# Kernel tuning notes

Measured on AMD Instinct MI355X. Metric: run time of the kernel, lower is better.

Reference implementation:

```python
import jax, jax.numpy as jnp
import numpy as np

ALPHA = 0.1
MAX_ITER = 35
TOL = 0.01
STEP = ALPHA / 2.0  # step_size = alpha/2 as in TV2DFunction.forward


def _prox_tv1d(step, y):
    """Exact 1D TV prox via taut-string lower/upper hulls (faithful port of _prox_tv1d)."""
    n = y.shape[0]
    width = n + 1
    dt = y.dtype
    cs = jnp.cumsum(y)
    y_low = jnp.concatenate([jnp.zeros(1, dt), cs - step]).at[width - 1].add(step)
    y_up = jnp.concatenate([jnp.zeros(1, dt), cs + step]).at[width - 1].add(-step)

    inf = jnp.asarray(jnp.inf, dt)
    il = jnp.zeros(width, jnp.int32)   # index_low
    iu = jnp.zeros(width, jnp.int32)   # index_up
    idx = jnp.zeros(width, jnp.int32)  # breakpoint indices
    sl = jnp.zeros(width, dt).at[0].set(inf)    # slope_low
    su = jnp.zeros(width, dt).at[0].set(-inf)   # slope_up
    z = jnp.zeros(width, dt)
    zero = jnp.int32(0)

    def fdiv(num, a, b):
        # a > b always holds on the taken branch; maximum() only guards the
        # unselected jnp.where branch against NaN/Inf.
        return num / jnp.maximum(a - b, 1).astype(dt)

    def body(i, st):
        il, sl, iu, su, idx, z, s_l, c_l, s_u, c_u, c = st
        c_l = c_l + 1
        c_u = c_u + 1
        il = il.at[c_l].set(i)
        iu = iu.at[c_u].set(i)
        sl = sl.at[c_l].set(y_low[i] - y_low[i - 1])

        def w1_cond(t):
            il_, sl_, c_l_ = t
            return (c_l_ > s_l + 1) & (sl_[jnp.maximum(s_l, c_l_ - 1)] <= sl_[c_l_])

        def w1_body(t):
            il_, sl_, c_l_ = t
            c_l_ = c_l_ - 1
            il_ = il_.at[c_l_].set(i)
            ns = jnp.where(c_l_ > s_l + 1,
                           fdiv(y_low[i] - y_low[il_[c_l_ - 1]], i, il_[c_l_ - 1]),
                           fdiv(y_low[i] - z[c], i, idx[c]))
            return il_, sl_.at[c_l_].set(ns), c_l_

        il, sl, c_l = jax.lax.while_loop(w1_cond, w1_body, (il, sl, c_l))

        su = su.at[c_u].set(y_up[i] - y_up[i - 1])

        def w2_cond(t):
            iu_, su_, c_u_ = t
            return (c_u_ > s_u + 1) & (su_[jnp.maximum(s_u, c_u_ - 1)] >= su_[c_u_])

        def w2_body(t):
            iu_, su_, c_u_ = t
            c_u_ = c_u_ - 1
            iu_ = iu_.at[c_u_].set(i)
            ns = jnp.where(c_u_ > s_u + 1,
                           fdiv(y_up[i] - y_up[iu_[c_u_ - 1]], i, iu_[c_u_ - 1]),
                           fdiv(y_up[i] - z[c], i, idx[c]))
            return iu_, su_.at[c_u_].set(ns), c_u_

        iu, su, c_u = jax.lax.while_loop(w2_cond, w2_body, (iu, su, c_u))

        def w3_cond(t):
            idx_, z_, sl_, il_, s_u_, c_ = t
            return (c_l == s_l + 1) & (c_u > s_u_ + 1) & (sl_[c_l] >= su[s_u_ + 1])

        def w3_body(t):
            idx_, z_, sl_, il_, s_u_, c_ = t
            c_ = c_ + 1
            s_u_ = s_u_ + 1
            k = iu[s_u_]
            idx_ = idx_.at[c_].set(k)
            z_ = z_.at[c_].set(y_up[k])
            il_ = il_.at[s_l].set(k)
            sl_ = sl_.at[c_l].set(fdiv(y_low[i] - y_up[k], i, k))
            return idx_, z_, sl_, il_, s_u_, c_

        idx, z, sl, il, s_u, c = jax.lax.while_loop(w3_cond, w3_body, (idx, z, sl, il, s_u, c))

        def w4_cond(t):
            idx_, z_, su_, iu_, s_l_, c_ = t
            return (c_u == s_u + 1) & (c_l > s_l_ + 1) & (su_[c_u] <= sl[s_l_ + 1])

        def w4_body(t):
            idx_, z_, su_, iu_, s_l_, c_ = t
            c_ = c_ + 1
            s_l_ = s_l_ + 1
            k = il[s_l_]
            idx_ = idx_.at[c_].set(k)
            z_ = z_.at[c_].set(y_low[k])
            iu_ = iu_.at[s_u].set(k)
            su_ = su_.at[c_u].set(fdiv(y_up[i] - y_low[k], i, k))
            return idx_, z_, su_, iu_, s_l_, c_

        idx, z, su, iu, s_l, c = jax.lax.while_loop(w4_cond, w4_body, (idx, z, su, iu, s_l, c))

        return il, sl, iu, su, idx, z, s_l, c_l, s_u, c_u, c

    st = (il, sl, iu, su, idx, z, zero, zero, zero, zero, zero)
    il, sl, iu, su, idx, z, s_l, c_l, s_u, c_u, c = jax.lax.fori_loop(1, width, body, st)

    # tail: append remaining lower-hull points to the breakpoint list
    m = c_l - s_l
    offs = jnp.arange(width)
    valid = (offs >= 1) & (offs <= m)
    src = il[jnp.clip(s_l + offs, 0, width - 1)]
    tgt = jnp.where(valid, c + offs, width)  # 'width' is out of bounds -> dropped
    idx = idx.at[tgt].set(src, mode='drop')
    z = z.at[tgt].set(y_low[src], mode='drop')
    c = c + m

    # piecewise-constant output: slope of taut string on each segment
    a = (z - jnp.roll(z, 1)) / jnp.maximum(idx - jnp.roll(idx, 1), 1).astype(dt)
    knots = jnp.where(offs <= c, idx, n + 1)  # sorted; idx[c] == n
    seg = jnp.searchsorted(knots, jnp.arange(n), side='right')  # segment id in [1, c]
    return a[seg]


def _prox_cols(step, A):
    return jax.vmap(lambda col: _prox_tv1d(step, col), in_axes=1, out_axes=1)(A)


def _prox_rows(step, A):
    return jax.vmap(lambda row: _prox_tv1d(step, row))(A)


def _prox_tv2d(x, step, max_iter, tol):
    """Douglas-Rachford splitting for 2D TV prox (Barbero & Sra 2014)."""
    def cond(carry):
        it, x_, p, q, acc = carry
        return (it < max_iter) & (acc >= tol)

    def body(carry):
        it, x_, p, q, _ = carry
        y = _prox_cols(step, x_ + p)
        p = p + x_ - y
        x2 = _prox_rows(step, y + q)
        q = q + y - x2
        acc = jnp.max(jnp.abs(y - x2))
        return it + 1, x2, p, q, acc

    z0 = jnp.zeros_like(x)
    init = (jnp.int32(0), x, z0, z0, jnp.asarray(jnp.inf, x.dtype))
    return jax.lax.while_loop(cond, body, init)[1]


def setup_inputs() -> dict:
    key = jax.random.key(0)
    X = jax.random.normal(key, (256, 256), dtype=jnp.float32)
    return {"X": X}


def reference(X):
    return _prox_tv2d(X, STEP, MAX_ITER, TOL)
```

## Files before the change

### kernel.cpp

```cpp
#include <hip/hip_runtime.h>

#define N 256
#define NLINE 4
#define NB (N / NLINE)
#define NT (NLINE * 64)
#define LAM 0.05f
#define TWOLAM (2.0f * LAM)
#define FOURLAM (4.0f * LAM)
#define MAXIT 35
#define TOL 0.01f
#define SLOTSTRIDE 16

__device__ __forceinline__ float rlane(float v, int lane) {
    return __int_as_float(__builtin_amdgcn_readlane(__float_as_int(v), lane));
}

__device__ __forceinline__ void gstore(float* p, float v) {
    __hip_atomic_store(p, v, __ATOMIC_RELAXED, __HIP_MEMORY_SCOPE_AGENT);
}
__device__ __forceinline__ float4 gload4(const float* p) {
    float4 r;
    asm volatile("global_load_dwordx4 %0, %1, off sc0 sc1\n\ts_waitcnt vmcnt(0)"
                 : "=&v"(r) : "v"(p) : "memory");
    return r;
}

struct Dist { float r0, r1, r2, r3; };

__device__ __forceinline__ float dfetch(const Dist& d, int k) {
    const int lane = k & 63;
    const int sel = k >> 6;
    float a = rlane(d.r0, lane);
    float b = rlane(d.r1, lane);
    float c = rlane(d.r2, lane);
    float e = rlane(d.r3, lane);
    float ab = (sel & 1) ? b : a;
    float ce = (sel & 1) ? e : c;
    return (sel & 2) ? ce : ab;
}

__device__ __forceinline__ void flushseg(Dist& o, int lo, int hi, float val, int lane) {
    const unsigned len = (unsigned)(hi - lo);
    const int base = lane - lo;
    o.r0 = ((unsigned)(base      ) <= len) ? val : o.r0;
    o.r1 = ((unsigned)(base + 64 ) <= len) ? val : o.r1;
    o.r2 = ((unsigned)(base + 128) <= len) ? val : o.r2;
    o.r3 = ((unsigned)(base + 192) <= len) ? val : o.r3;
}

__device__ __forceinline__ unsigned long long sel4(unsigned long long a, unsigned long long b,
                                                   unsigned long long c, unsigned long long d, int r) {
    unsigned long long ab = (r & 1) ? b : a;
    unsigned long long cd = (r & 1) ? d : c;
    return (r & 2) ? cd : ab;
}

__device__ void tv1d_scan(const Dist& v, Dist& o, const int lane)
{
    const float lam = LAM, mlam = -LAM, twolam = TWOLAM;

    Dist vnx;
    {
        float a0 = __shfl_down(v.r0, 1), a1 = __shfl_down(v.r1, 1);
        float a2 = __shfl_down(v.r2, 1), a3 = __shfl_down(v.r3, 1);
        const bool hi = (lane == 63);
        vnx.r0 = hi ? rlane(v.r1, 0) : a0;
        vnx.r1 = hi ? rlane(v.r2, 0) : a1;
        vnx.r2 = hi ? rlane(v.r3, 0) : a2;
        vnx.r3 = hi ? v.r3 : a3;
    }
    Dist d;
    d.r0 = vnx.r0 - v.r0;  d.r1 = vnx.r1 - v.r1;
    d.r2 = vnx.r2 - v.r2;  d.r3 = vnx.r3 - v.r3;
    const unsigned lambits = __float_as_uint(lam);
    Dist sl;
    sl.r0 = __uint_as_float((__float_as_uint(d.r0) & 0x80000000u) | lambits);
    sl.r1 = __uint_as_float((__float_as_uint(d.r1) & 0x80000000u) | lambits);
    sl.r2 = __uint_as_float((__float_as_uint(d.r2) & 0x80000000u) | lambits);
    sl.r3 = __uint_as_float((__float_as_uint(d.r3) & 0x80000000u) | lambits);
    Dist slp;
    {
        float b0 = __shfl_up(sl.r0, 1), b1 = __shfl_up(sl.r1, 1);
        float b2 = __shfl_up(sl.r2, 1), b3 = __shfl_up(sl.r3, 1);
        const bool lo = (lane == 0);
        slp.r0 = lo ? 0.0f : b0;
        slp.r1 = lo ? rlane(sl.r0, 63) : b1;
        slp.r2 = lo ? rlane(sl.r1, 63) : b2;
        slp.r3 = lo ? rlane(sl.r2, 63) : b3;
    }
    Dist e, g;
    {
        float t0 = v.r0 - slp.r0, t1 = v.r1 - slp.r1, t2 = v.r2 - slp.r2, t3 = v.r3 - slp.r3;
        e.r0 = t0 + sl.r0;  e.r1 = t1 + sl.r1;  e.r2 = t2 + sl.r2;  e.r3 = t3 + sl.r3;
        g.r0 = t0 - lam;    g.r1 = t1 - lam;    g.r2 = t2 - lam;    g.r3 = t3 - lam;
    }
    const unsigned long long S0 = __ballot(d.r0 < 0.0f);
    const unsigned long long S1 = __ballot(d.r1 < 0.0f);
    const unsigned long long S2 = __ballot(d.r2 < 0.0f);
    const unsigned long long S3 = __ballot(d.r3 < 0.0f);
    const unsigned long long B20 = __ballot(fabsf(d.r0) > TWOLAM);
    const unsigned long long B21 = __ballot(fabsf(d.r1) > TWOLAM);
    const unsigned long long B22 = __ballot(fabsf(d.r2) > TWOLAM);
    const unsigned long long B23 = __ballot(fabsf(d.r3) > TWOLAM);
    const unsigned long long B40 = __ballot(fabsf(d.r0) > FOURLAM);
    const unsigned long long B41 = __ballot(fabsf(d.r1) > FOURLAM);
    const unsigned long long B42 = __ballot(fabsf(d.r2) > FOURLAM);
    const unsigned long long B43 = __ballot(fabsf(d.r3) > FOURLAM);
    const unsigned long long Sp0 = (S0 << 1);
    const unsigned long long Sp1 = (S1 << 1) | (S0 >> 63);
    const unsigned long long Sp2 = (S2 << 1) | (S1 >> 63);
    const unsigned long long Sp3 = (S3 << 1) | (S2 >> 63);
    const unsigned long long NF0 = ~(B40 | (B20 & ~(S0 ^ Sp0)));
    const unsigned long long NF1 = ~(B41 | (B21 & ~(S1 ^ Sp1)));
    const unsigned long long NF2 = ~(B42 | (B22 & ~(S2 ^ Sp2)));
    const unsigned long long NF3 = ~((B43 | (B23 & ~(S3 ^ Sp3))) & 0x7FFFFFFFFFFFFFFFull);
    const unsigned long long FNn0 = (S0 & B20) | (~S0 & B40);
    const unsigned long long FNn1 = (S1 & B21) | (~S1 & B41);
    const unsigned long long FNn2 = (S2 & B22) | (~S2 & B42);
    const unsigned long long FNn3 = (S3 & B23) | (~S3 & B43);
    const unsigned long long FNp0 = (~S0 & B20) | (S0 & B40);
    const unsigned long long FNp1 = (~S1 & B21) | (S1 & B41);
    const unsigned long long FNp2 = (~S2 & B22) | (S2 & B42);
    const unsigned long long FNp3 = (~S3 & B23) | (S3 & B43);
    const int initFF = (int)(B40 & 1ull);

    auto firstnf = [&](int jmin) -> int {
        const int w = jmin >> 6;
        unsigned long long m = sel4(NF0, NF1, NF2, NF3, w) >> (jmin & 63);
        if (m) return jmin + (int)__builtin_ctzll(m);
        unsigned long long m1 = (w < 1) ? NF1 : 0ull;
        unsigned long long m2 = (w < 2) ? NF2 : 0ull;
        if (m1) return 64 + (int)__builtin_ctzll(m1);
        if (m2) return 128 + (int)__builtin_ctzll(m2);
        return 192 + (int)__builtin_ctzll(NF3);
    };

    auto trigbit = [&](int kk, int neg) -> int {
        const int w = kk >> 6;
        const unsigned long long m = neg ? sel4(FNn0, FNn1, FNn2, FNn3, w)
                                         : sel4(FNp0, FNp1, FNp2, FNp3, w);
        return (int)((m >> (kk & 63)) & 1ull);
    };

    int k = 0, k0 = 0, km = 0, kp = 0;
    float umin = lam, umax = mlam;
    const float v0 = rlane(v.r0, 0);
    float vmin = v0 - lam, vmax = v0 + lam;
    float flen = 1.0f;
    float rnext = 0.5f;
    float vn1 = rlane(vnx.r0, 0);

    auto fastfwd = [&]() {
        const int K1 = firstnf(k + 1);
        const int sneg = (int)((sel4(S0, S1, S2, S3, k >> 6) >> (k & 63)) & 1ull);
        flushseg(o, k, k, sneg ? vmin : vmax, lane);
        if (K1 > k + 1) {
            const int lo = k + 1;
            const unsigned len = (unsigned)(K1 - 1 - lo);
            const int base = lane - lo;
            o.r0 = ((unsigned)(base      ) <= len) ? e.r0 : o.r0;
            o.r1 = ((unsigned)(base + 64 ) <= len) ? e.r1 : o.r1;
            o.r2 = ((unsigned)(base + 128) <= len) ? e.r2 : o.r2;
            o.r3 = ((unsigned)(base + 192) <= len) ? e.r3 : o.r3;
        }
        k = K1; k0 = K1; km = K1; kp = K1;
        vmin = dfetch(g, K1);
        vmax = vmin + twolam;
        umin = lam; umax = mlam;
        flen = 1.0f; rnext = 0.5f;
        vn1 = dfetch(vnx, K1);
    };

    auto do_step = [&]() {
        const float un = umin + vn1 - vmin;
        const float ux = umax + vn1 - vmax;
        const bool neg = un < mlam;
        const bool pos = ux > lam;
        const int wn = (k + 1) >> 6, bn = (k + 1) & 63;
        const int tn = (int)((sel4(FNn0, FNn1, FNn2, FNn3, wn) >> bn) & 1ull);
        const int tp = (int)((sel4(FNp0, FNp1, FNp2, FNp3, wn) >> bn) & 1ull);
        if (__builtin_expect((int)(neg | pos), 1)) {
            const float fval = neg ? vmin : vmax;
            const int   fhi  = neg ? km : kp;
            flushseg(o, k0, fhi, fval, lane);
            const int k0n = fhi + 1;
            float vstar;
            int trig;
            if (__builtin_expect((int)(k0n <= k), 0)) {
                vstar = dfetch(v, k0n);
                trig = trigbit(k0n, (int)neg);
            } else {
                vstar = vn1;
                trig = neg ? tn : tp;
            }
            k = k0n; k0 = k0n; km = k0n; kp = k0n;
            vmin = neg ? vstar : vstar - twolam;
            vmax = vmin + twolam;
            umin = lam; umax = mlam;
            flen = 1.0f; rnext = 0.5f;
            if (k < N - 1 && trig) {
                fastfwd();
            } else {
                vn1 = dfetch(vnx, k);
            }
        } else {
            k++;
            const float r = rnext;
            flen += 1.0f;
            const bool cmin = (un >= lam);
            const bool cmax = (ux <= mlam);
            vmin = cmin ? fmaf(un - lam, r, vmin) : vmin;
            km   = cmin ? k : km;
            umin = cmin ? lam : un;
            vmax = cmax ? fmaf(ux + lam, r, vmax) : vmax;
            kp   = cmax ? k : kp;
            umax = cmax ? mlam : ux;
            vn1 = dfetch(vnx, k);
            rnext = __builtin_amdgcn_rcpf(flen + 1.0f);
        }
    };

    if (initFF) fastfwd();

    for (;;) {
        while (k < N - 1) {
            do_step();
            if (k >= N - 1) break;
            do_step();
        }
        for (;;) {
            if (umin < 0.0f) {
                flushseg(o, k0, km, vmin, lane);
                k0 = km + 1;
                if (k0 > N - 1) return;
                km = k = k0;
                vmin = dfetch(v, k0);
                umin = lam;
                umax = vmin + lam - vmax;
                flen = 1.0f;
            } else if (umax > 0.0f) {
                flushseg(o, k0, kp, vmax, lane);
                k0 = kp + 1;
                if (k0 > N - 1) return;
                kp = k = k0;
                vmax = dfetch(v, k0);
                umax = mlam;
                umin = vmax - lam - vmin;
                flen = 1.0f;
            } else {
                vmin += umin / flen;
                flushseg(o, k0, k, vmin, lane);
                return;
            }
            if (k != N - 1) break;
        }
        rnext = 0.5f;
        vn1 = dfetch(vnx, k);
    }
}

__device__ __forceinline__ void gridbar1(unsigned long long* slots, unsigned seq,
                                         unsigned accfill, int t) {
    __syncthreads();
    __builtin_amdgcn_s_waitcnt(0);
    if (t == 0)
        __hip_atomic_store(&slots[blockIdx.x * SLOTSTRIDE],
                           ((unsigned long long)accfill << 32) | (unsigned long long)seq,
                           __ATOMIC_RELAXED, __HIP_MEMORY_SCOPE_AGENT);
    if (t < 64) {
        unsigned long long f = __hip_atomic_load(&slots[t * SLOTSTRIDE],
                                                 __ATOMIC_RELAXED, __HIP_MEMORY_SCOPE_AGENT);
        for (;;) {
            unsigned long long fn = __hip_atomic_load(&slots[t * SLOTSTRIDE],
                                                      __ATOMIC_RELAXED, __HIP_MEMORY_SCOPE_AGENT);
            if (__all((int)((unsigned)f >= seq))) break;
            f = fn;
        }
    }
    __syncthreads();
}

__device__ __forceinline__ void gridbar2(unsigned long long* slots, unsigned seq,
                                         unsigned acc, int t, int* s_dec) {
    __syncthreads();
    __builtin_amdgcn_s_waitcnt(0);
    if (t == 0)
        __hip_atomic_store(&slots[blockIdx.x * SLOTSTRIDE],
                           ((unsigned long long)acc << 32) | (unsigned long long)seq,
                           __ATOMIC_RELAXED, __HIP_MEMORY_SCOPE_AGENT);
    if (t < 64) {
        unsigned long long f = __hip_atomic_load(&slots[t * SLOTSTRIDE],
                                                 __ATOMIC_RELAXED, __HIP_MEMORY_SCOPE_AGENT);
        for (;;) {
            unsigned long long fn = __hip_atomic_load(&slots[t * SLOTSTRIDE],
                                                      __ATOMIC_RELAXED, __HIP_MEMORY_SCOPE_AGENT);
            if (__all((int)((unsigned)f >= seq))) break;
            f = fn;
        }
        unsigned a = (unsigned)(f >> 32);
        #pragma unroll
        for (int off = 32; off > 0; off >>= 1) {
            unsigned aa = __shfl_xor(a, off);
            a = (aa > a) ? aa : a;
        }
        if (t == 0) *s_dec = (__uint_as_float(a) < TOL) ? 1 : 0;
    }
    __syncthreads();
}

__global__ __launch_bounds__(NT) void tv2d_coop(const float* __restrict__ X,
                                                float* __restrict__ xw,
                                                float* __restrict__ y,
                                                unsigned long long* __restrict__ slots)
{
    const int t = threadIdx.x;
    const int lane = t & 63;
    const int wave = t >> 6;
    const int line = blockIdx.x * NLINE + wave;
    const int col4 = 4 * blockIdx.x;
    __shared__ float tile[N * 5];
    __shared__ unsigned s_acc;
    __shared__ int s_dec;
    if (t == 0) s_acc = 0u;

    Dist p = {0.f, 0.f, 0.f, 0.f};
    Dist q = {0.f, 0.f, 0.f, 0.f};
    unsigned accprev = 0u;

    for (int it = 0; it < MAXIT; ++it) {
        const float* xs = (it == 0) ? X : xw;
        const float4 xc = gload4(xs + t * N + col4);
        tile[t * 5 + 0] = xc.x;
        tile[t * 5 + 1] = xc.y;
        tile[t * 5 + 2] = xc.z;
        tile[t * 5 + 3] = xc.w;
        __syncthreads();
        Dist v, o;
        v.r0 = tile[(lane      ) * 5 + wave] + p.r0;
        v.r1 = tile[(lane + 64 ) * 5 + wave] + p.r1;
        v.r2 = tile[(lane + 128) * 5 + wave] + p.r2;
        v.r3 = tile[(lane + 192) * 5 + wave] + p.r3;
        tv1d_scan(v, o, lane);
        p.r0 = v.r0 - o.r0;  p.r1 = v.r1 - o.r1;
        p.r2 = v.r2 - o.r2;  p.r3 = v.r3 - o.r3;
        float* yt = y + line * N;
        gstore(yt + lane,       o.r0);
        gstore(yt + lane + 64,  o.r1);
        gstore(yt + lane + 128, o.r2);
        gstore(yt + lane + 192, o.r3);
        gridbar1(slots, 2u * (unsigned)it + 1u, accprev, t);

        const float4 yc = gload4(y + t * N + col4);
        tile[t * 5 + 0] = yc.x;
        tile[t * 5 + 1] = yc.y;
        tile[t * 5 + 2] = yc.z;
        tile[t * 5 + 3] = yc.w;
        __syncthreads();
        float y0 = tile[(lane      ) * 5 + wave];
        float y1 = tile[(lane + 64 ) * 5 + wave];
        float y2 = tile[(lane + 128) * 5 + wave];
        float y3 = tile[(lane + 192) * 5 + wave];
        Dist w, o2;
        w.r0 = y0 + q.r0;
        w.r1 = y1 + q.r1;
        w.r2 = y2 + q.r2;
        w.r3 = y3 + q.r3;
        tv1d_scan(w, o2, lane);
        float d0 = y0 - o2.r0;
        float d1 = y1 - o2.r1;
        float d2 = y2 - o2.r2;
        float d3 = y3 - o2.r3;
        q.r0 = w.r0 - o2.r0;  q.r1 = w.r1 - o2.r1;
        q.r2 = w.r2 - o2.r2;  q.r3 = w.r3 - o2.r3;
        float* xr = xw + line * N;
        gstore(xr + lane,       o2.r0);
        gstore(xr + lane + 64,  o2.r1);
        gstore(xr + lane + 128, o2.r2);
        gstore(xr + lane + 192, o2.r3);

        float am = fmaxf(fmaxf(fabsf(d0), fabsf(d1)), fmaxf(fabsf(d2), fabsf(d3)));
        #pragma unroll
        for (int off = 32; off > 0; off >>= 1)
            am = fmaxf(am, __shfl_xor(am, off));
        if (lane == 0) atomicMax(&s_acc, __float_as_uint(am));
        __syncthreads();
        const unsigned ba = s_acc;

        if (it == MAXIT - 1) break;

        gridbar2(slots, 2u * (unsigned)it + 2u, ba, t, &s_dec);
        if (t == 0) s_acc = 0u;
        if (s_dec) break;
        accprev = ba;
    }
}

extern "C" void kernel_launch(void* const* d_in, const int* in_sizes, int n_in,
                              void* d_out, int out_size, void* d_ws, size_t ws_size,
                              hipStream_t stream) {
    const float* X = (const float*)d_in[0];
    float* xw = (float*)d_out;
    float* y = (float*)d_ws;
    unsigned long long* slots = (unsigned long long*)((char*)d_ws + (size_t)N * N * sizeof(float));
    (void)hipMemsetAsync((void*)slots, 0, NB * SLOTSTRIDE * sizeof(unsigned long long), stream);
    void* args[] = { (void*)&X, (void*)&xw, (void*)&y, (void*)&slots };
    (void)hipLaunchCooperativeKernel((void*)tv2d_coop, dim3(NB), dim3(NT), args, 0, stream);
}
```

Measured before the change: 285.2 us.

## Replace block-level grid barriers with per-wave slots, DPP reductions, prefetched scan loads

Each wave now publishes its own slot in the grid barrier. Wave 0 polls all 256 slots and releases the other waves of its block through a shared-memory flag, instead of the barrier being wrapped in two __syncthreads. The per-wave max reductions switch from shuffle loops to DPP row operations plus a readlane, which removes the shared atomicMax and a block sync. The scan step also computes the next-element register selects for all three branch targets up front, to shorten the dependency chain after the branch. The cost is more slot polling traffic per wave and extra select work on every scan step.

```diff
diff --git a/kernel.cpp b/kernel.cpp
--- a/kernel.cpp
+++ b/kernel.cpp
@@ -9,7 +9,7 @@
 #define FOURLAM (4.0f * LAM)
 #define MAXIT 35
 #define TOL 0.01f
-#define SLOTSTRIDE 16
+#define SLOTSTRIDE 4
 
 __device__ __forceinline__ float rlane(float v, int lane) {
     return __int_as_float(__builtin_amdgcn_readlane(__float_as_int(v), lane));
@@ -53,6 +53,17 @@
     unsigned long long ab = (r & 1) ? b : a;
     unsigned long long cd = (r & 1) ? d : c;
     return (r & 2) ? cd : ab;
+}
+
+__device__ __forceinline__ unsigned wredmax(unsigned x) {
+    unsigned t;
+    t = (unsigned)__builtin_amdgcn_update_dpp(0, (int)x, 0x111, 0xf, 0xf, true); x = x > t ? x : t;
+    t = (unsigned)__builtin_amdgcn_update_dpp(0, (int)x, 0x112, 0xf, 0xf, true); x = x > t ? x : t;
+    t = (unsigned)__builtin_amdgcn_update_dpp(0, (int)x, 0x114, 0xf, 0xf, true); x = x > t ? x : t;
+    t = (unsigned)__builtin_amdgcn_update_dpp(0, (int)x, 0x118, 0xf, 0xf, true); x = x > t ? x : t;
+    t = (unsigned)__builtin_amdgcn_update_dpp(0, (int)x, 0x142, 0xf, 0xf, true); x = x > t ? x : t;
+    t = (unsigned)__builtin_amdgcn_update_dpp(0, (int)x, 0x143, 0xf, 0xf, true); x = x > t ? x : t;
+    return (unsigned)__builtin_amdgcn_readlane((int)x, 63);
 }
 
 __device__ void tv1d_scan(const Dist& v, Dist& o, const int lane)
@@ -172,6 +183,9 @@
     };
 
     auto do_step = [&]() {
+        const float pf_nj = dfetch(vnx, k + 1);
+        const float pf_n  = dfetch(vnx, km + 1);
+        const float pf_p  = dfetch(vnx, kp + 1);
         const float un = umin + vn1 - vmin;
         const float ux = umax + vn1 - vmax;
         const bool neg = un < mlam;
@@ -201,7 +215,7 @@
             if (k < N - 1 && trig) {
                 fastfwd();
             } else {
-                vn1 = dfetch(vnx, k);
+                vn1 = neg ? pf_n : pf_p;
             }
         } else {
             k++;
@@ -215,7 +229,7 @@
             vmax = cmax ? fmaf(ux + lam, r, vmax) : vmax;
             kp   = cmax ? k : kp;
             umax = cmax ? mlam : ux;
-            vn1 = dfetch(vnx, k);
+            vn1 = pf_nj;
             rnext = __builtin_amdgcn_rcpf(flen + 1.0f);
         }
     };
@@ -259,53 +273,48 @@
     }
 }
 
-__device__ __forceinline__ void gridbar1(unsigned long long* slots, unsigned seq,
-                                         unsigned accfill, int t) {
-    __syncthreads();
+template <bool WANT>
+__device__ __forceinline__ unsigned wavebar(unsigned long long* slots, unsigned seq,
+                                            unsigned payload, int line, int lane, int wave,
+                                            unsigned long long* s_rel)
+{
     __builtin_amdgcn_s_waitcnt(0);
-    if (t == 0)
-        __hip_atomic_store(&slots[blockIdx.x * SLOTSTRIDE],
-                           ((unsigned long long)accfill << 32) | (unsigned long long)seq,
-                           __ATOMIC_RELAXED, __HIP_MEMORY_SCOPE_AGENT);
-    if (t < 64) {
-        unsigned long long f = __hip_atomic_load(&slots[t * SLOTSTRIDE],
-                                                 __ATOMIC_RELAXED, __HIP_MEMORY_SCOPE_AGENT);
+    __hip_atomic_store(&slots[line * SLOTSTRIDE],
+                       ((unsigned long long)payload << 32) | (unsigned long long)seq,
+                       __ATOMIC_RELAXED, __HIP_MEMORY_SCOPE_AGENT);
+    unsigned ga = 0u;
+    if (wave == 0) {
+        auto ld = [&](int i) {
+            return __hip_atomic_load(&slots[i * SLOTSTRIDE],
+                                     __ATOMIC_RELAXED, __HIP_MEMORY_SCOPE_AGENT);
+        };
+        unsigned long long f0 = ld(lane), f1 = ld(lane + 64),
+                           f2 = ld(lane + 128), f3 = ld(lane + 192);
         for (;;) {
-            unsigned long long fn = __hip_atomic_load(&slots[t * SLOTSTRIDE],
-                                                      __ATOMIC_RELAXED, __HIP_MEMORY_SCOPE_AGENT);
-            if (__all((int)((unsigned)f >= seq))) break;
-            f = fn;
-        }
-    }
-    __syncthreads();
-}
-
-__device__ __forceinline__ void gridbar2(unsigned long long* slots, unsigned seq,
-                                         unsigned acc, int t, int* s_dec) {
-    __syncthreads();
-    __builtin_amdgcn_s_waitcnt(0);
-    if (t == 0)
-        __hip_atomic_store(&slots[blockIdx.x * SLOTSTRIDE],
-                           ((unsigned long long)acc << 32) | (unsigned long long)seq,
-                           __ATOMIC_RELAXED, __HIP_MEMORY_SCOPE_AGENT);
-    if (t < 64) {
-        unsigned long long f = __hip_atomic_load(&slots[t * SLOTSTRIDE],
-                                                 __ATOMIC_RELAXED, __HIP_MEMORY_SCOPE_AGENT);
-        for (;;) {
-            unsigned long long fn = __hip_atomic_load(&slots[t * SLOTSTRIDE],
-                                                      __ATOMIC_RELAXED, __HIP_MEMORY_SCOPE_AGENT);
-            if (__all((int)((unsigned)f >= seq))) break;
-            f = fn;
-        }
-        unsigned a = (unsigned)(f >> 32);
-        #pragma unroll
-        for (int off = 32; off > 0; off >>= 1) {
-            unsigned aa = __shfl_xor(a, off);
-            a = (aa > a) ? aa : a;
-        }
-        if (t == 0) *s_dec = (__uint_as_float(a) < TOL) ? 1 : 0;
-    }
-    __syncthreads();
+            unsigned long long g0 = ld(lane), g1 = ld(lane + 64),
+                               g2 = ld(lane + 128), g3 = ld(lane + 192);
+            const bool ok = ((unsigned)f0 >= seq) & ((unsigned)f1 >= seq) &
+                            ((unsigned)f2 >= seq) & ((unsigned)f3 >= seq);
+            if (__all((int)ok)) break;
+            f0 = g0; f1 = g1; f2 = g2; f3 = g3;
+        }
+        if (WANT) {
+            unsigned a = (unsigned)(f0 >> 32), b = (unsigned)(f1 >> 32);
+            unsigned c = (unsigned)(f2 >> 32), d = (unsigned)(f3 >> 32);
+            a = a > b ? a : b;  c = c > d ? c : d;  a = a > c ? a : c;
+            ga = wredmax(a);
+        }
+        if (lane == 0)
+            __hip_atomic_store(s_rel, ((unsigned long long)ga << 32) | (unsigned long long)seq,
+                               __ATOMIC_RELAXED, __HIP_MEMORY_SCOPE_WORKGROUP);
+    } else {
+        unsigned long long r;
+        do {
+            r = __hip_atomic_load(s_rel, __ATOMIC_RELAXED, __HIP_MEMORY_SCOPE_WORKGROUP);
+        } while ((unsigned)r < seq);
+        if (WANT) ga = (unsigned)(r >> 32);
+    }
+    return ga;
 }
 
 __global__ __launch_bounds__(NT) void tv2d_coop(const float* __restrict__ X,
@@ -319,9 +328,8 @@
     const int line = blockIdx.x * NLINE + wave;
     const int col4 = 4 * blockIdx.x;
     __shared__ float tile[N * 5];
-    __shared__ unsigned s_acc;
-    __shared__ int s_dec;
-    if (t == 0) s_acc = 0u;
+    __shared__ unsigned long long s_rel;
+    if (t == 0) s_rel = 0ull;
 
     Dist p = {0.f, 0.f, 0.f, 0.f};
     Dist q = {0.f, 0.f, 0.f, 0.f};
@@ -348,7 +356,7 @@
         gstore(yt + lane + 64,  o.r1);
         gstore(yt + lane + 128, o.r2);
         gstore(yt + lane + 192, o.r3);
-        gridbar1(slots, 2u * (unsigned)it + 1u, accprev, t);
+        wavebar<false>(slots, 2u * (unsigned)it + 1u, accprev, line, lane, wave, &s_rel);
 
         const float4 yc = gload4(y + t * N + col4);
         tile[t * 5 + 0] = yc.x;
@@ -379,19 +387,13 @@
         gstore(xr + lane + 192, o2.r3);
 
         float am = fmaxf(fmaxf(fabsf(d0), fabsf(d1)), fmaxf(fabsf(d2), fabsf(d3)));
-        #pragma unroll
-        for (int off = 32; off > 0; off >>= 1)
-            am = fmaxf(am, __shfl_xor(am, off));
-        if (lane == 0) atomicMax(&s_acc, __float_as_uint(am));
-        __syncthreads();
-        const unsigned ba = s_acc;
+        const unsigned acc = wredmax(__float_as_uint(am));
 
         if (it == MAXIT - 1) break;
 
-        gridbar2(slots, 2u * (unsigned)it + 2u, ba, t, &s_dec);
-        if (t == 0) s_acc = 0u;
-        if (s_dec) break;
-        accprev = ba;
+        const unsigned ga = wavebar<true>(slots, 2u * (unsigned)it + 2u, acc, line, lane, wave, &s_rel);
+        if (__uint_as_float(ga) < TOL) break;
+        accprev = acc;
     }
 }
 
@@ -402,7 +404,7 @@
     float* xw = (float*)d_out;
     float* y = (float*)d_ws;
     unsigned long long* slots = (unsigned long long*)((char*)d_ws + (size_t)N * N * sizeof(float));
-    (void)hipMemsetAsync((void*)slots, 0, NB * SLOTSTRIDE * sizeof(unsigned long long), stream);
+    (void)hipMemsetAsync((void*)slots, 0, N * SLOTSTRIDE * sizeof(unsigned long long), stream);
     void* args[] = { (void*)&X, (void*)&xw, (void*)&y, (void*)&slots };
     (void)hipLaunchCooperativeKernel((void*)tv2d_coop, dim3(NB), dim3(NT), args, 0, stream);
 }
```

After: 310.9 us. 1.09x slower.
